# Performance work log

Hardware: AMD Instinct MI355X
Metric: run time of the kernel (lower is better)

## Reference

```python
import jax, jax.numpy as jnp
import numpy as np

D, H, S, L = 512, 8, 4, 2
HD = D // H          # 64 head dim
F = 4 * D            # 2048 FFN hidden
EPS = 1e-5


def setup_inputs() -> dict:
    key = jax.random.key(0)
    ks = jax.random.split(key, 26)
    B = 16384
    w = 0.02
    inp = {
        'text_pattern':   jax.random.normal(ks[0], (B, D), jnp.float32),
        'text_semantic':  jax.random.normal(ks[1], (B, D), jnp.float32),
        'image_pattern':  jax.random.normal(ks[2], (B, D), jnp.float32),
        'image_semantic': jax.random.normal(ks[3], (B, D), jnp.float32),
        # per-(layer, stream) attention projections, stacked [L,S,...]
        'Wq': jax.random.normal(ks[4], (L, S, D, D), jnp.float32) * w,
        'bq': jnp.zeros((L, S, D), jnp.float32),
        'Wk': jax.random.normal(ks[5], (L, S, D, D), jnp.float32) * w,
        'bk': jnp.zeros((L, S, D), jnp.float32),
        'Wv': jax.random.normal(ks[6], (L, S, D, D), jnp.float32) * w,
        'bv': jnp.zeros((L, S, D), jnp.float32),
        'Wo': jax.random.normal(ks[7], (L, S, D, D), jnp.float32) * w,
        'bo': jnp.zeros((L, S, D), jnp.float32),
        'ln_g': jnp.ones((L, S, D), jnp.float32),
        'ln_b': jnp.zeros((L, S, D), jnp.float32),
        'W1': jax.random.normal(ks[8], (L, S, D, F), jnp.float32) * w,
        'b1': jnp.zeros((L, S, F), jnp.float32),
        'W2': jax.random.normal(ks[9], (L, S, F, D), jnp.float32) * w,
        'b2': jnp.zeros((L, S, D), jnp.float32),
        # final fusion MLP: 4*D -> 2*D -> D
        'Wf1': jax.random.normal(ks[10], (S * D, 2 * D), jnp.float32) * w,
        'bf1': jnp.zeros((2 * D,), jnp.float32),
        'Wf2': jax.random.normal(ks[11], (2 * D, D), jnp.float32) * w,
        'bf2': jnp.zeros((D,), jnp.float32),
    }
    return inp


def _layer_norm(x, g, b):
    # x: [B,S,D], g/b: [S,D]; normalize over last dim
    mu = jnp.mean(x, axis=-1, keepdims=True)
    var = jnp.mean(jnp.square(x - mu), axis=-1, keepdims=True)
    return (x - mu) * jax.lax.rsqrt(var + EPS) * g + b


def reference(text_pattern, text_semantic, image_pattern, image_semantic,
              Wq, bq, Wk, bk, Wv, bv, Wo, bo, ln_g, ln_b,
              W1, b1, W2, b2, Wf1, bf1, Wf2, bf2):
    # streams stacked: [B, S=4, D]; each stream's query_len is 1, keys are all 4 streams
    x = jnp.stack([text_pattern, text_semantic, image_pattern, image_semantic], axis=1)
    B = x.shape[0]
    attn0 = None
    for l in range(L):
        # per-stream query projection of its own token: [B,S,D]
        q = jnp.einsum('bsd,sde->bse', x, Wq[l]) + bq[l]
        # per-stream K/V projections of ALL streams: [B,S(query-stream),K(key-pos),D]
        k = jnp.einsum('bkd,sde->bske', x, Wk[l]) + bk[l][:, None, :]
        v = jnp.einsum('bkd,sde->bske', x, Wv[l]) + bv[l][:, None, :]
        qh = q.reshape(B, S, H, HD)
        kh = k.reshape(B, S, S, H, HD)
        vh = v.reshape(B, S, S, H, HD)
        scores = jnp.einsum('bshe,bskhe->bshk', qh, kh) / (HD ** 0.5)  # [B,S,H,K]
        w = jax.nn.softmax(scores, axis=-1)
        ctx = jnp.einsum('bshk,bskhe->bshe', w, vh).reshape(B, S, D)
        attn_out = jnp.einsum('bsd,sde->bse', ctx, Wo[l]) + bo[l]
        if l == 0:
            attn0 = w  # [B,S,H,K]: layer-0 attention weights per stream
        h = _layer_norm(x + attn_out, ln_g[l], ln_b[l])
        ffn = jnp.einsum('bsf,sfd->bsd',
                         jax.nn.relu(jnp.einsum('bsd,sdf->bsf', h, W1[l]) + b1[l]),
                         W2[l]) + b2[l]
        x = h + ffn
    concat = x.reshape(B, S * D)
    fused = jax.nn.relu(concat @ Wf1 + bf1) @ Wf2 + bf2  # [B, D]
    return fused, attn0
```

## Files before the change

kernel.cpp:

```cpp
#include <hip/hip_runtime.h>
#include <stdint.h>

typedef unsigned short u16;
typedef __bf16 bf16x8 __attribute__((ext_vector_type(8)));
typedef float f32x4 __attribute__((ext_vector_type(4)));

constexpr int NB = 16384;
constexpr int DM = 512;
constexpr int NS = 4;
constexpr int FH = 2048;
constexpr int XW = NS * DM;
constexpr float EPSL = 1e-5f;

__device__ __forceinline__ float bf2f(u16 u) { return __uint_as_float(((uint32_t)u) << 16); }
__device__ __forceinline__ u16 f2bf(float f) {
  uint32_t u = __float_as_uint(f);
  u += 0x7fffu + ((u >> 16) & 1u);
  return (u16)(u >> 16);
}
__device__ __forceinline__ void unpack8(uint4 p, float* f) {
  f[0] = __uint_as_float(p.x << 16); f[1] = __uint_as_float(p.x & 0xffff0000u);
  f[2] = __uint_as_float(p.y << 16); f[3] = __uint_as_float(p.y & 0xffff0000u);
  f[4] = __uint_as_float(p.z << 16); f[5] = __uint_as_float(p.z & 0xffff0000u);
  f[6] = __uint_as_float(p.w << 16); f[7] = __uint_as_float(p.w & 0xffff0000u);
}
__device__ __forceinline__ uint4 pack8(const float* f) {
  uint4 r;
  r.x = (uint32_t)f2bf(f[0]) | ((uint32_t)f2bf(f[1]) << 16);
  r.y = (uint32_t)f2bf(f[2]) | ((uint32_t)f2bf(f[3]) << 16);
  r.z = (uint32_t)f2bf(f[4]) | ((uint32_t)f2bf(f[5]) << 16);
  r.w = (uint32_t)f2bf(f[6]) | ((uint32_t)f2bf(f[7]) << 16);
  return r;
}
__device__ __forceinline__ void gl_lds16(const void* g, void* l) {
  __builtin_amdgcn_global_load_lds((const __attribute__((address_space(1))) void*)g,
                                   (__attribute__((address_space(3))) void*)l, 16, 0, 0);
}

__device__ __forceinline__ void xcd_remap(int& bx, int& by) {
  const int flat = blockIdx.y * 128 + blockIdx.x;
  const int xcd = flat & 7;
  const int t = flat >> 3;
  bx = xcd * 16 + (t & 15);
  by = t >> 4;
}

__device__ __forceinline__ void gemm_cv(
    const u16* __restrict__ A, int lda,
    const u16* __restrict__ Bt, int K,
    u16* As, u16* Bs, f32x4 (&acc)[4][4], int bx, int by)
{
  const int tid = threadIdx.x;
  const int ln = tid & 63;
  const int w  = tid >> 6;
  const int wm = w >> 1, wn = w & 1;
  const int m0 = bx * 128;
  const int n0 = by * 128;
  const int grow = ln >> 2;
  const int gcol = ((ln & 3) ^ ((ln >> 3) & 3)) * 8;
  const u16* Ab = A  + (size_t)(m0 + w * 32 + grow) * lda + gcol;
  const u16* Bb = Bt + (size_t)(n0 + w * 32 + grow) * K   + gcol;

  auto stage = [&](int buf, int k0) {
#pragma unroll
    for (int i = 0; i < 2; ++i) {
      gl_lds16(Ab + (size_t)i * 16 * lda + k0, &As[buf * 4096 + (w * 32 + i * 16) * 32]);
      gl_lds16(Bb + (size_t)i * 16 * K   + k0, &Bs[buf * 4096 + (w * 32 + i * 16) * 32]);
    }
  };

  __syncthreads();
  const int nt = K >> 5;
  stage(0, 0);
  if (nt > 1) {
    stage(1, 32);
    asm volatile("s_waitcnt vmcnt(4)" ::: "memory");
  } else {
    asm volatile("s_waitcnt vmcnt(0)" ::: "memory");
  }
  __builtin_amdgcn_s_barrier();
  asm volatile("" ::: "memory");

  const int rx = ((ln & 15) >> 1) & 3;
  const int qb = ln >> 4;
  const int cb = (qb ^ rx) * 8;
  int cur = 0, nxt2 = 2;
  for (int t = 0; t < nt; ++t) {
    bf16x8 af[4], bfv[4];
#pragma unroll
    for (int m = 0; m < 4; ++m) {
      af[m]  = *(const bf16x8*)&As[cur * 4096 + (wm * 64 + m * 16 + (ln & 15)) * 32 + cb];
      bfv[m] = *(const bf16x8*)&Bs[cur * 4096 + (wn * 64 + m * 16 + (ln & 15)) * 32 + cb];
    }
#pragma unroll
    for (int m = 0; m < 4; ++m)
#pragma unroll
      for (int n = 0; n < 4; ++n)
        acc[m][n] = __builtin_amdgcn_mfma_f32_16x16x32_bf16(af[m], bfv[n], acc[m][n], 0, 0, 0);
    if (t + 2 < nt) {
      stage(nxt2, (t + 2) * 32);
      asm volatile("s_waitcnt vmcnt(4)" ::: "memory");
      __builtin_amdgcn_s_barrier();
      asm volatile("" ::: "memory");
    } else if (t + 1 < nt) {
      asm volatile("s_waitcnt vmcnt(0)" ::: "memory");
      __builtin_amdgcn_s_barrier();
      asm volatile("" ::: "memory");
    }
    cur = cur + 1;  if (cur == 3)  cur = 0;
    nxt2 = nxt2 + 1; if (nxt2 == 3) nxt2 = 0;
  }
  asm volatile("" ::: "memory");
}

template<bool RELU, bool RESID, bool OUTF32>
__global__ __launch_bounds__(256) void k_gemm(
    const u16* __restrict__ A, int lda, long aZ,
    const u16* __restrict__ Bt, long bZ,
    const float* __restrict__ bias, long biasZ,
    const u16* __restrict__ Rsd, int ldr, long rZ,
    void* __restrict__ Cp, int ldc, long cZ, int K)
{
  const int z = blockIdx.z;
  A += (long)z * aZ; Bt += (long)z * bZ; bias += (long)z * biasZ;
  int bx, by; xcd_remap(bx, by);
  __shared__ alignas(16) u16 As[3 * 4096];
  __shared__ alignas(16) u16 Bs[3 * 4096];
  f32x4 acc[4][4] = {};
  gemm_cv(A, lda, Bt, K, As, Bs, acc, bx, by);
  const int ln = threadIdx.x & 63;
  const int w = threadIdx.x >> 6;
  const int wm = w >> 1, wn = w & 1;
  const int m0 = bx * 128, n0 = by * 128;
#pragma unroll
  for (int n = 0; n < 4; ++n) {
    const int gc = n0 + wn * 64 + n * 16 + (ln & 15);
    const float bv = bias[gc];
#pragma unroll
    for (int m = 0; m < 4; ++m) {
#pragma unroll
      for (int j = 0; j < 4; ++j) {
        const int gr = m0 + wm * 64 + m * 16 + (ln >> 4) * 4 + j;
        float v = acc[m][n][j] + bv;
        if constexpr (RESID) v += bf2f(Rsd[(long)z * rZ + (size_t)gr * ldr + gc]);
        if constexpr (RELU)  v = v > 0.f ? v : 0.f;
        if constexpr (OUTF32) ((float*)Cp)[(long)z * cZ + (size_t)gr * ldc + gc] = v;
        else                  ((u16*)Cp)[(long)z * cZ + (size_t)gr * ldc + gc] = f2bf(v);
      }
    }
  }
}

__global__ __launch_bounds__(256) void k_kdot(
    const u16* __restrict__ xcat, const u16* __restrict__ WkT_l,
    const u16* __restrict__ Qb, float* __restrict__ wbuf)
{
  const int s = blockIdx.z >> 2, kp = blockIdx.z & 3;
  int bx, by; xcd_remap(bx, by);
  __shared__ alignas(16) u16 As[3 * 4096];
  __shared__ alignas(16) u16 Bs[3 * 4096];
  f32x4 acc[4][4] = {};
  gemm_cv(xcat + kp * DM, XW, WkT_l + (size_t)s * DM * DM, DM, As, Bs, acc, bx, by);
  const int ln = threadIdx.x & 63;
  const int w = threadIdx.x >> 6;
  const int wm = w >> 1, wn = w & 1;
  const int m0 = bx * 128, n0 = by * 128;
  const int h = (n0 >> 6) + wn;
  float p[4][4];
#pragma unroll
  for (int m = 0; m < 4; ++m)
#pragma unroll
    for (int j = 0; j < 4; ++j) p[m][j] = 0.f;
#pragma unroll
  for (int n = 0; n < 4; ++n) {
    const int gc = n0 + wn * 64 + n * 16 + (ln & 15);
#pragma unroll
    for (int m = 0; m < 4; ++m) {
#pragma unroll
      for (int j = 0; j < 4; ++j) {
        const int gr = m0 + wm * 64 + m * 16 + (ln >> 4) * 4 + j;
        p[m][j] += acc[m][n][j] * bf2f(Qb[((size_t)s * NB + gr) * DM + gc]);
      }
    }
  }
#pragma unroll
  for (int m = 0; m < 4; ++m)
#pragma unroll
    for (int j = 0; j < 4; ++j) {
      float v = p[m][j];
      v += __shfl_xor(v, 1, 64);
      v += __shfl_xor(v, 2, 64);
      v += __shfl_xor(v, 4, 64);
      v += __shfl_xor(v, 8, 64);
      p[m][j] = v;
    }
  if ((ln & 15) == 0) {
#pragma unroll
    for (int m = 0; m < 4; ++m)
#pragma unroll
      for (int j = 0; j < 4; ++j) {
        const int gr = m0 + wm * 64 + m * 16 + (ln >> 4) * 4 + j;
        wbuf[(((size_t)s * NB + gr) * 8 + h) * 4 + kp] = p[m][j] * 0.125f;
      }
  }
}

__global__ __launch_bounds__(256) void k_gemmv4(
    const u16* __restrict__ xcat, const u16* __restrict__ WvT_l,
    const float* __restrict__ bv_l, const float* __restrict__ wbuf,
    u16* __restrict__ ctxc)
{
  int bx, by; xcd_remap(bx, by);
  __shared__ alignas(16) u16 As[3 * 4096];
  __shared__ alignas(16) u16 Bs[3 * 4096];
  const int ln = threadIdx.x & 63;
  const int w = threadIdx.x >> 6;
  const int wm = w >> 1, wn = w & 1;
  const int m0 = bx * 128, n0 = by * 128;
  const int s  = n0 >> 9;
  const int hh = ((n0 >> 6) + wn) & 7;
  f32x4 facc[4][4] = {};
  for (int kp = 0; kp < 4; ++kp) {
    f32x4 acc[4][4] = {};
    gemm_cv(xcat + kp * DM, XW, WvT_l, DM, As, Bs, acc, bx, by);
    float wv[4][4];
#pragma unroll
    for (int m = 0; m < 4; ++m)
#pragma unroll
      for (int j = 0; j < 4; ++j) {
        const int gr = m0 + wm * 64 + m * 16 + (ln >> 4) * 4 + j;
        wv[m][j] = wbuf[(((size_t)s * NB + gr) * 8 + hh) * 4 + kp];
      }
#pragma unroll
    for (int n = 0; n < 4; ++n) {
      const float bvv = bv_l[n0 + wn * 64 + n * 16 + (ln & 15)];
#pragma unroll
      for (int m = 0; m < 4; ++m)
#pragma unroll
        for (int j = 0; j < 4; ++j)
          facc[m][n][j] += (acc[m][n][j] + bvv) * wv[m][j];
    }
  }
#pragma unroll
  for (int n = 0; n < 4; ++n) {
    const int gc = n0 + wn * 64 + n * 16 + (ln & 15);
#pragma unroll
    for (int m = 0; m < 4; ++m)
#pragma unroll
      for (int j = 0; j < 4; ++j) {
        const int gr = m0 + wm * 64 + m * 16 + (ln >> 4) * 4 + j;
        ctxc[(size_t)gr * XW + gc] = f2bf(facc[m][n][j]);
      }
  }
}

__global__ __launch_bounds__(256) void k_softmax(
    float* __restrict__ wbuf, float* __restrict__ a0)
{
  const int t = blockIdx.x * 256 + threadIdx.x;
  float4 v = ((const float4*)wbuf)[t];
  const float mx = fmaxf(fmaxf(v.x, v.y), fmaxf(v.z, v.w));
  float4 e;
  e.x = __expf(v.x - mx); e.y = __expf(v.y - mx);
  e.z = __expf(v.z - mx); e.w = __expf(v.w - mx);
  const float inv = 1.f / (e.x + e.y + e.z + e.w);
  e.x *= inv; e.y *= inv; e.z *= inv; e.w *= inv;
  ((float4*)wbuf)[t] = e;
  if (a0 != nullptr) {
    const int s = t >> 17, b = (t >> 3) & (NB - 1), h = t & 7;
    ((float4*)a0)[((size_t)b * NS + s) * 8 + h] = e;
  }
}

__global__ __launch_bounds__(256) void k_ln(
    u16* __restrict__ xcat, const float* __restrict__ g, const float* __restrict__ bb)
{
  const int ln = threadIdx.x & 63;
  const int row = blockIdx.x * 4 + (threadIdx.x >> 6);
  const int b = row >> 2, s = row & 3;
  u16* p = xcat + (size_t)b * XW + s * DM;
  float v[8];
  { uint4 t = ((const uint4*)p)[ln]; unpack8(t, v); }
  float sum = 0.f;
#pragma unroll
  for (int j = 0; j < 8; ++j) sum += v[j];
#pragma unroll
  for (int off = 1; off < 64; off <<= 1) sum += __shfl_xor(sum, off, 64);
  const float mu = sum * (1.f / DM);
  float s2 = 0.f;
#pragma unroll
  for (int j = 0; j < 8; ++j) { float d = v[j] - mu; s2 += d * d; }
#pragma unroll
  for (int off = 1; off < 64; off <<= 1) s2 += __shfl_xor(s2, off, 64);
  const float rs = rsqrtf(s2 * (1.f / DM) + EPSL);
  const int e0 = s * DM + ln * 8;
  float o[8];
#pragma unroll
  for (int j = 0; j < 8; ++j) o[j] = (v[j] - mu) * rs * g[e0 + j] + bb[e0 + j];
  ((uint4*)p)[ln] = pack8(o);
}

__global__ void k_pack(const float* __restrict__ t0, const float* __restrict__ t1,
                       const float* __restrict__ t2, const float* __restrict__ t3,
                       u16* __restrict__ xcat)
{
  const int total = NB * XW / 8;
  for (int t = blockIdx.x * blockDim.x + threadIdx.x; t < total; t += gridDim.x * blockDim.x) {
    const int b = t >> 8;
    const int r = t & 255;
    const int s = r >> 6;
    const int d0 = (r & 63) * 8;
    const float* p = (s == 0) ? t0 : (s == 1) ? t1 : (s == 2) ? t2 : t3;
    float f[8];
#pragma unroll
    for (int j = 0; j < 8; ++j) f[j] = p[(size_t)b * DM + d0 + j];
    ((uint4*)xcat)[t] = pack8(f);
  }
}

__global__ void k_tcvt(const float* __restrict__ src, u16* __restrict__ dst,
                       int rlog, int clog, int nb)
{
  const int mlog = rlog + clog;
  const size_t total = (size_t)nb << mlog;
  for (size_t t = (size_t)blockIdx.x * blockDim.x + threadIdx.x; t < total;
       t += (size_t)gridDim.x * blockDim.x) {
    const size_t mat = t >> mlog;
    const uint32_t rem = (uint32_t)(t & ((1u << mlog) - 1));
    const uint32_t n = rem >> rlog;
    const uint32_t r = rem & ((1u << rlog) - 1);
    dst[t] = f2bf(src[(mat << mlog) + ((size_t)r << clog) + n]);
  }
}

extern "C" void kernel_launch(void* const* d_in, const int* in_sizes, int n_in,
                              void* d_out, int out_size, void* d_ws, size_t ws_size,
                              hipStream_t stream)
{
  (void)in_sizes; (void)n_in; (void)out_size;
  const float* t0  = (const float*)d_in[0];
  const float* t1  = (const float*)d_in[1];
  const float* t2  = (const float*)d_in[2];
  const float* t3  = (const float*)d_in[3];
  const float* Wq  = (const float*)d_in[4];
  const float* bq  = (const float*)d_in[5];
  const float* Wk  = (const float*)d_in[6];
  const float* Wv  = (const float*)d_in[8];
  const float* bv  = (const float*)d_in[9];
  const float* Wo  = (const float*)d_in[10];
  const float* bo  = (const float*)d_in[11];
  const float* lng = (const float*)d_in[12];
  const float* lnb = (const float*)d_in[13];
  const float* W1  = (const float*)d_in[14];
  const float* b1  = (const float*)d_in[15];
  const float* W2  = (const float*)d_in[16];
  const float* b2  = (const float*)d_in[17];
  const float* Wf1 = (const float*)d_in[18];
  const float* bf1 = (const float*)d_in[19];
  const float* Wf2 = (const float*)d_in[20];
  const float* bf2 = (const float*)d_in[21];

  size_t off = 0;
  char* ws = (char*)d_ws;
  auto take = [&](size_t n) { char* p = ws + off; off += (n + 255) & ~(size_t)255; return p; };
  u16* WqT  = (u16*)take(8ull * DM * DM * 2);
  u16* WkT  = (u16*)take(8ull * DM * DM * 2);
  u16* WvT  = (u16*)take(8ull * DM * DM * 2);
  u16* WoT  = (u16*)take(8ull * DM * DM * 2);
  u16* W1T  = (u16*)take(8ull * DM * FH * 2);
  u16* W2T  = (u16*)take(8ull * FH * DM * 2);
  u16* Wf1T = (u16*)take((size_t)XW * 1024 * 2);
  u16* Wf2T = (u16*)take((size_t)1024 * DM * 2);
  u16* xcat = (u16*)take((size_t)NB * XW * 2);
  char* U1  = take((size_t)NB * XW * 2);
  float* wbuf = (float*)take(4ull * NB * 8 * 4 * 4);
  const size_t needed = off;

  u16* Qb   = (u16*)U1;
  u16* ctxc = (u16*)U1;
  u16* ffn1 = (u16*)U1;
  u16* y1   = (u16*)U1;
  float* attn0 = (float*)d_out + (size_t)NB * DM;

  if (needed > ws_size) return;

  k_tcvt<<<dim3(1024), dim3(256), 0, stream>>>(Wq, WqT, 9, 9, 8);
  k_tcvt<<<dim3(1024), dim3(256), 0, stream>>>(Wk, WkT, 9, 9, 8);
  k_tcvt<<<dim3(1024), dim3(256), 0, stream>>>(Wv, WvT, 9, 9, 8);
  k_tcvt<<<dim3(1024), dim3(256), 0, stream>>>(Wo, WoT, 9, 9, 8);
  k_tcvt<<<dim3(1024), dim3(256), 0, stream>>>(W1, W1T, 9, 11, 8);
  k_tcvt<<<dim3(1024), dim3(256), 0, stream>>>(W2, W2T, 11, 9, 8);
  k_tcvt<<<dim3(1024), dim3(256), 0, stream>>>(Wf1, Wf1T, 11, 10, 1);
  k_tcvt<<<dim3(1024), dim3(256), 0, stream>>>(Wf2, Wf2T, 10, 9, 1);
  k_pack<<<dim3(2048), dim3(256), 0, stream>>>(t0, t1, t2, t3, xcat);

  const size_t WSQ = (size_t)DM * DM;
  for (int ly = 0; ly < 2; ++ly) {
    const u16* WqT_l = WqT + (size_t)ly * 4 * WSQ;
    const u16* WkT_l = WkT + (size_t)ly * 4 * WSQ;
    const u16* WvT_l = WvT + (size_t)ly * 4 * WSQ;
    const u16* WoT_l = WoT + (size_t)ly * 4 * WSQ;
    k_gemm<false, false, false><<<dim3(128, 4, 4), dim3(256), 0, stream>>>(
        xcat, XW, DM, WqT_l, WSQ, bq + (size_t)ly * XW, DM,
        nullptr, 0, 0, Qb, DM, (long)NB * DM, DM);
    k_kdot<<<dim3(128, 4, 16), dim3(256), 0, stream>>>(xcat, WkT_l, Qb, wbuf);
    k_softmax<<<dim3(4 * NB * 8 / 256), dim3(256), 0, stream>>>(
        wbuf, (ly == 0) ? attn0 : (float*)nullptr);
    k_gemmv4<<<dim3(128, 16), dim3(256), 0, stream>>>(
        xcat, WvT_l, bv + (size_t)ly * XW, wbuf, ctxc);
    k_gemm<false, true, false><<<dim3(128, 4, 4), dim3(256), 0, stream>>>(
        ctxc, XW, DM, WoT_l, WSQ, bo + (size_t)ly * XW, DM,
        xcat, XW, DM, xcat, XW, DM, DM);
    k_ln<<<dim3(NB), dim3(256), 0, stream>>>(xcat, lng + ly * XW, lnb + ly * XW);
    for (int s = 0; s < NS; ++s) {
      const size_t wsl = (size_t)(ly * 4 + s);
      k_gemm<true, false, false><<<dim3(128, 16, 1), dim3(256), 0, stream>>>(
          xcat + s * DM, XW, 0, W1T + wsl * (size_t)DM * FH, 0, b1 + wsl * FH, 0,
          nullptr, 0, 0, ffn1, FH, 0, DM);
      k_gemm<false, true, false><<<dim3(128, 4, 1), dim3(256), 0, stream>>>(
          ffn1, FH, 0, W2T + wsl * (size_t)FH * DM, 0, b2 + wsl * DM, 0,
          xcat + s * DM, XW, 0, xcat + s * DM, XW, 0, FH);
    }
  }
  k_gemm<true, false, false><<<dim3(128, 8, 1), dim3(256), 0, stream>>>(
      xcat, XW, 0, Wf1T, 0, bf1, 0, nullptr, 0, 0, y1, 1024, 0, XW);
  k_gemm<false, false, true><<<dim3(128, 4, 1), dim3(256), 0, stream>>>(
      y1, 1024, 0, Wf2T, 0, bf2, 0, nullptr, 0, 0, d_out, DM, 0, 1024);
}
```

Baseline: 2.551 ms.

## Switch GEMM core to BK=64 double-buffered MFMA-fragment LDS layout and tiled transposes

The shared GEMM mainloop changes from a triple-buffered BK=32 swizzled layout to a double-buffered BK=64 layout. Tiles are stored in LDS directly in MFMA fragment order, so each lane reads contiguous 16-byte chunks and the barrier count per K step is halved. The block-index remap is generalized to include the z dimension so batched launches are also spread across XCDs. The weight transpose-convert kernel becomes a 32x32 LDS-tiled transpose with coalesced reads and writes. In exchange, LDS per block grows and the pipeline is shallower, with a full vmcnt(0) wait before every barrier.

After: 3.483 ms. 36.5% more time.

```diff
diff --git a/kernel.cpp b/kernel.cpp
--- a/kernel.cpp
+++ b/kernel.cpp
@@ -37,15 +37,19 @@
                                    (__attribute__((address_space(3))) void*)l, 16, 0, 0);
 }
 
-__device__ __forceinline__ void xcd_remap(int& bx, int& by) {
-  const int flat = blockIdx.y * 128 + blockIdx.x;
-  const int xcd = flat & 7;
-  const int t = flat >> 3;
-  bx = xcd * 16 + (t & 15);
-  by = t >> 4;
-}
-
-__device__ __forceinline__ void gemm_cv(
+__device__ __forceinline__ void remap(int& bx, int& by, int& bz) {
+  const int gx = gridDim.x, gy = gridDim.y;
+  const int fl = (blockIdx.z * gy + blockIdx.y) * gx + blockIdx.x;
+  const int xcd = fl & 7;
+  const int t = fl >> 3;
+  const int bw = gx >> 3;
+  bx = xcd * bw + t % bw;
+  const int u = t / bw;
+  by = u % gy;
+  bz = u / gy;
+}
+
+__device__ __forceinline__ void gemm64(
     const u16* __restrict__ A, int lda,
     const u16* __restrict__ Bt, int K,
     u16* As, u16* Bs, f32x4 (&acc)[4][4], int bx, int by)
@@ -56,59 +60,54 @@
   const int wm = w >> 1, wn = w & 1;
   const int m0 = bx * 128;
   const int n0 = by * 128;
-  const int grow = ln >> 2;
-  const int gcol = ((ln & 3) ^ ((ln >> 3) & 3)) * 8;
-  const u16* Ab = A  + (size_t)(m0 + w * 32 + grow) * lda + gcol;
-  const u16* Bb = Bt + (size_t)(n0 + w * 32 + grow) * K   + gcol;
+  const u16* Ab = A  + (size_t)(m0 + w * 16 + (ln & 15)) * lda + ((ln >> 4) & 3) * 8;
+  const u16* Bb = Bt + (size_t)(n0 + w * 16 + (ln & 15)) * K   + ((ln >> 4) & 3) * 8;
 
   auto stage = [&](int buf, int k0) {
 #pragma unroll
-    for (int i = 0; i < 2; ++i) {
-      gl_lds16(Ab + (size_t)i * 16 * lda + k0, &As[buf * 4096 + (w * 32 + i * 16) * 32]);
-      gl_lds16(Bb + (size_t)i * 16 * K   + k0, &Bs[buf * 4096 + (w * 32 + i * 16) * 32]);
-    }
+    for (int kk = 0; kk < 2; ++kk)
+#pragma unroll
+      for (int i = 0; i < 2; ++i) {
+        gl_lds16(Ab + (size_t)(i * 64) * lda + k0 + kk * 32,
+                 &As[buf * 8192 + ((kk * 8 + i * 4 + w) * 512) + ln * 8]);
+        gl_lds16(Bb + (size_t)(i * 64) * K + k0 + kk * 32,
+                 &Bs[buf * 8192 + ((kk * 8 + i * 4 + w) * 512) + ln * 8]);
+      }
   };
 
   __syncthreads();
-  const int nt = K >> 5;
+  const int nt = K >> 6;
   stage(0, 0);
-  if (nt > 1) {
-    stage(1, 32);
-    asm volatile("s_waitcnt vmcnt(4)" ::: "memory");
-  } else {
-    asm volatile("s_waitcnt vmcnt(0)" ::: "memory");
-  }
+  asm volatile("s_waitcnt vmcnt(0)" ::: "memory");
   __builtin_amdgcn_s_barrier();
   asm volatile("" ::: "memory");
 
-  const int rx = ((ln & 15) >> 1) & 3;
-  const int qb = ln >> 4;
-  const int cb = (qb ^ rx) * 8;
-  int cur = 0, nxt2 = 2;
+  int buf = 0;
   for (int t = 0; t < nt; ++t) {
-    bf16x8 af[4], bfv[4];
-#pragma unroll
-    for (int m = 0; m < 4; ++m) {
-      af[m]  = *(const bf16x8*)&As[cur * 4096 + (wm * 64 + m * 16 + (ln & 15)) * 32 + cb];
-      bfv[m] = *(const bf16x8*)&Bs[cur * 4096 + (wn * 64 + m * 16 + (ln & 15)) * 32 + cb];
-    }
-#pragma unroll
-    for (int m = 0; m < 4; ++m)
-#pragma unroll
-      for (int n = 0; n < 4; ++n)
-        acc[m][n] = __builtin_amdgcn_mfma_f32_16x16x32_bf16(af[m], bfv[n], acc[m][n], 0, 0, 0);
-    if (t + 2 < nt) {
-      stage(nxt2, (t + 2) * 32);
-      asm volatile("s_waitcnt vmcnt(4)" ::: "memory");
-      __builtin_amdgcn_s_barrier();
-      asm volatile("" ::: "memory");
-    } else if (t + 1 < nt) {
-      asm volatile("s_waitcnt vmcnt(0)" ::: "memory");
-      __builtin_amdgcn_s_barrier();
-      asm volatile("" ::: "memory");
-    }
-    cur = cur + 1;  if (cur == 3)  cur = 0;
-    nxt2 = nxt2 + 1; if (nxt2 == 3) nxt2 = 0;
+    if (t + 1 < nt) stage(buf ^ 1, (t + 1) * 64);
+    bf16x8 af[4][2], bfv[4][2];
+#pragma unroll
+    for (int kk = 0; kk < 2; ++kk) {
+#pragma unroll
+      for (int mf = 0; mf < 4; ++mf)
+        af[mf][kk] = *(const bf16x8*)&As[buf * 8192 + (kk * 8 + wm * 4 + mf) * 512 + ln * 8];
+#pragma unroll
+      for (int nf = 0; nf < 4; ++nf)
+        bfv[nf][kk] = *(const bf16x8*)&Bs[buf * 8192 + (kk * 8 + wn * 4 + nf) * 512 + ln * 8];
+    }
+#pragma unroll
+    for (int kk = 0; kk < 2; ++kk)
+#pragma unroll
+      for (int mf = 0; mf < 4; ++mf)
+#pragma unroll
+        for (int nf = 0; nf < 4; ++nf)
+          acc[mf][nf] = __builtin_amdgcn_mfma_f32_16x16x32_bf16(
+              af[mf][kk], bfv[nf][kk], acc[mf][nf], 0, 0, 0);
+    if (t + 1 == nt) break;
+    asm volatile("s_waitcnt vmcnt(0)" ::: "memory");
+    __builtin_amdgcn_s_barrier();
+    asm volatile("" ::: "memory");
+    buf ^= 1;
   }
   asm volatile("" ::: "memory");
 }
@@ -121,31 +120,30 @@
     const u16* __restrict__ Rsd, int ldr, long rZ,
     void* __restrict__ Cp, int ldc, long cZ, int K)
 {
-  const int z = blockIdx.z;
-  A += (long)z * aZ; Bt += (long)z * bZ; bias += (long)z * biasZ;
-  int bx, by; xcd_remap(bx, by);
-  __shared__ alignas(16) u16 As[3 * 4096];
-  __shared__ alignas(16) u16 Bs[3 * 4096];
+  int bx, by, bz; remap(bx, by, bz);
+  A += (long)bz * aZ; Bt += (long)bz * bZ; bias += (long)bz * biasZ;
+  __shared__ alignas(16) u16 As[2 * 8192];
+  __shared__ alignas(16) u16 Bs[2 * 8192];
   f32x4 acc[4][4] = {};
-  gemm_cv(A, lda, Bt, K, As, Bs, acc, bx, by);
+  gemm64(A, lda, Bt, K, As, Bs, acc, bx, by);
   const int ln = threadIdx.x & 63;
   const int w = threadIdx.x >> 6;
   const int wm = w >> 1, wn = w & 1;
   const int m0 = bx * 128, n0 = by * 128;
 #pragma unroll
-  for (int n = 0; n < 4; ++n) {
-    const int gc = n0 + wn * 64 + n * 16 + (ln & 15);
+  for (int nf = 0; nf < 4; ++nf) {
+    const int gc = n0 + wn * 64 + nf * 16 + (ln & 15);
     const float bv = bias[gc];
 #pragma unroll
-    for (int m = 0; m < 4; ++m) {
+    for (int mf = 0; mf < 4; ++mf) {
 #pragma unroll
       for (int j = 0; j < 4; ++j) {
-        const int gr = m0 + wm * 64 + m * 16 + (ln >> 4) * 4 + j;
-        float v = acc[m][n][j] + bv;
-        if constexpr (RESID) v += bf2f(Rsd[(long)z * rZ + (size_t)gr * ldr + gc]);
+        const int gr = m0 + wm * 64 + mf * 16 + (ln >> 4) * 4 + j;
+        float v = acc[mf][nf][j] + bv;
+        if constexpr (RESID) v += bf2f(Rsd[(long)bz * rZ + (size_t)gr * ldr + gc]);
         if constexpr (RELU)  v = v > 0.f ? v : 0.f;
-        if constexpr (OUTF32) ((float*)Cp)[(long)z * cZ + (size_t)gr * ldc + gc] = v;
-        else                  ((u16*)Cp)[(long)z * cZ + (size_t)gr * ldc + gc] = f2bf(v);
+        if constexpr (OUTF32) ((float*)Cp)[(long)bz * cZ + (size_t)gr * ldc + gc] = v;
+        else                  ((u16*)Cp)[(long)bz * cZ + (size_t)gr * ldc + gc] = f2bf(v);
       }
     }
   }
@@ -155,12 +153,12 @@
     const u16* __restrict__ xcat, const u16* __restrict__ WkT_l,
     const u16* __restrict__ Qb, float* __restrict__ wbuf)
 {
-  const int s = blockIdx.z >> 2, kp = blockIdx.z & 3;
-  int bx, by; xcd_remap(bx, by);
-  __shared__ alignas(16) u16 As[3 * 4096];
-  __shared__ alignas(16) u16 Bs[3 * 4096];
+  int bx, by, bz; remap(bx, by, bz);
+  const int s = bz >> 2, kp = bz & 3;
+  __shared__ alignas(16) u16 As[2 * 8192];
+  __shared__ alignas(16) u16 Bs[2 * 8192];
   f32x4 acc[4][4] = {};
-  gemm_cv(xcat + kp * DM, XW, WkT_l + (size_t)s * DM * DM, DM, As, Bs, acc, bx, by);
+  gemm64(xcat + kp * DM, XW, WkT_l + (size_t)s * DM * DM, DM, As, Bs, acc, bx, by);
   const int ln = threadIdx.x & 63;
   const int w = threadIdx.x >> 6;
   const int wm = w >> 1, wn = w & 1;
@@ -210,9 +208,9 @@
     const float* __restrict__ bv_l, const float* __restrict__ wbuf,
     u16* __restrict__ ctxc)
 {
-  int bx, by; xcd_remap(bx, by);
-  __shared__ alignas(16) u16 As[3 * 4096];
-  __shared__ alignas(16) u16 Bs[3 * 4096];
+  int bx, by, bz; remap(bx, by, bz); (void)bz;
+  __shared__ alignas(16) u16 As[2 * 8192];
+  __shared__ alignas(16) u16 Bs[2 * 8192];
   const int ln = threadIdx.x & 63;
   const int w = threadIdx.x >> 6;
   const int wm = w >> 1, wn = w & 1;
@@ -222,7 +220,7 @@
   f32x4 facc[4][4] = {};
   for (int kp = 0; kp < 4; ++kp) {
     f32x4 acc[4][4] = {};
-    gemm_cv(xcat + kp * DM, XW, WvT_l, DM, As, Bs, acc, bx, by);
+    gemm64(xcat + kp * DM, XW, WvT_l, DM, As, Bs, acc, bx, by);
     float wv[4][4];
 #pragma unroll
     for (int m = 0; m < 4; ++m)
@@ -318,19 +316,20 @@
   }
 }
 
-__global__ void k_tcvt(const float* __restrict__ src, u16* __restrict__ dst,
-                       int rlog, int clog, int nb)
-{
-  const int mlog = rlog + clog;
-  const size_t total = (size_t)nb << mlog;
-  for (size_t t = (size_t)blockIdx.x * blockDim.x + threadIdx.x; t < total;
-       t += (size_t)gridDim.x * blockDim.x) {
-    const size_t mat = t >> mlog;
-    const uint32_t rem = (uint32_t)(t & ((1u << mlog) - 1));
-    const uint32_t n = rem >> rlog;
-    const uint32_t r = rem & ((1u << rlog) - 1);
-    dst[t] = f2bf(src[(mat << mlog) + ((size_t)r << clog) + n]);
-  }
+__global__ __launch_bounds__(256) void k_tcvt(
+    const float* __restrict__ src, u16* __restrict__ dst, int R, int C)
+{
+  __shared__ float tl[32][33];
+  const int cx = blockIdx.x * 32, ry = blockIdx.y * 32;
+  const size_t base = (size_t)blockIdx.z * R * C;
+  const int lx = threadIdx.x & 31, ly = threadIdx.x >> 5;
+#pragma unroll
+  for (int i = 0; i < 32; i += 8)
+    tl[ly + i][lx] = src[base + (size_t)(ry + ly + i) * C + cx + lx];
+  __syncthreads();
+#pragma unroll
+  for (int i = 0; i < 32; i += 8)
+    dst[base + (size_t)(cx + ly + i) * R + ry + lx] = f2bf(tl[lx][ly + i]);
 }
 
 extern "C" void kernel_launch(void* const* d_in, const int* in_sizes, int n_in,
@@ -384,17 +383,17 @@
 
   if (needed > ws_size) return;
 
-  k_tcvt<<<dim3(1024), dim3(256), 0, stream>>>(Wq, WqT, 9, 9, 8);
-  k_tcvt<<<dim3(1024), dim3(256), 0, stream>>>(Wk, WkT, 9, 9, 8);
-  k_tcvt<<<dim3(1024), dim3(256), 0, stream>>>(Wv, WvT, 9, 9, 8);
-  k_tcvt<<<dim3(1024), dim3(256), 0, stream>>>(Wo, WoT, 9, 9, 8);
-  k_tcvt<<<dim3(1024), dim3(256), 0, stream>>>(W1, W1T, 9, 11, 8);
-  k_tcvt<<<dim3(1024), dim3(256), 0, stream>>>(W2, W2T, 11, 9, 8);
-  k_tcvt<<<dim3(1024), dim3(256), 0, stream>>>(Wf1, Wf1T, 11, 10, 1);
-  k_tcvt<<<dim3(1024), dim3(256), 0, stream>>>(Wf2, Wf2T, 10, 9, 1);
+  k_tcvt<<<dim3(16, 16, 8), dim3(256), 0, stream>>>(Wq, WqT, DM, DM);
+  k_tcvt<<<dim3(16, 16, 8), dim3(256), 0, stream>>>(Wk, WkT, DM, DM);
+  k_tcvt<<<dim3(16, 16, 8), dim3(256), 0, stream>>>(Wv, WvT, DM, DM);
+  k_tcvt<<<dim3(16, 16, 8), dim3(256), 0, stream>>>(Wo, WoT, DM, DM);
+  k_tcvt<<<dim3(64, 16, 8), dim3(256), 0, stream>>>(W1, W1T, DM, FH);
+  k_tcvt<<<dim3(16, 64, 8), dim3(256), 0, stream>>>(W2, W2T, FH, DM);
+  k_tcvt<<<dim3(32, 64, 1), dim3(256), 0, stream>>>(Wf1, Wf1T, XW, 1024);
+  k_tcvt<<<dim3(16, 32, 1), dim3(256), 0, stream>>>(Wf2, Wf2T, 1024, DM);
   k_pack<<<dim3(2048), dim3(256), 0, stream>>>(t0, t1, t2, t3, xcat);
 
-  const size_t WSQ = (size_t)DM * DM;
+  const long WSQ = (long)DM * DM;
   for (int ly = 0; ly < 2; ++ly) {
     const u16* WqT_l = WqT + (size_t)ly * 4 * WSQ;
     const u16* WkT_l = WkT + (size_t)ly * 4 * WSQ;
```
